# Optimization experiments

Hardware: AMD Instinct MI355X
Metric: run time of the kernel (lower is better)

## Reference

```python
import jax, jax.numpy as jnp
import numpy as np

N, D = 2048, 1024
OUT = 65536
S = 16384  # number of LSH-selected neurons


def setup_inputs() -> dict:
    key = jax.random.key(0)
    k1, k2, k3, k4 = jax.random.split(key, 4)
    x = jax.random.normal(k1, (N, D), dtype=jnp.float32)
    # original init: uniform(-1, 1) weights, zero bias; use randn-scale weights per spec
    weight = jax.random.normal(k2, (OUT, D), dtype=jnp.float32)
    bias = jax.random.normal(k3, (OUT,), dtype=jnp.float32)
    sample_ids = jax.random.randint(k4, (S,), 0, OUT, dtype=jnp.int64)
    return {"x": x, "weight": weight, "bias": bias, "sample_ids": sample_ids}


def reference(x, weight, bias, sample_ids):
    # Gather selected neuron rows (F.embedding equivalent)
    sample_weights = weight[sample_ids]          # [S, D]
    sample_bias = bias[sample_ids]               # [S]
    # x @ W_sel.T + b_sel  -> [N, S]
    sample_logits = jnp.einsum('nd,sd->ns', x, sample_weights) + sample_bias
    return sample_logits
```

## Files before the change

### kernel.cpp

```cpp
#include <hip/hip_runtime.h>
#include <stdint.h>


typedef __bf16 bf16x8 __attribute__((ext_vector_type(8)));
typedef float f32x4 __attribute__((ext_vector_type(4)));

#define BM 256
#define BN 256
#define BK 64

__device__ __forceinline__ ushort f2bf(float f) {
  union { float f; uint32_t u; } c; c.f = f;
  uint32_t u = c.u;
  return (ushort)((u + 0x7FFFu + ((u >> 16) & 1u)) >> 16);
}

__global__ __launch_bounds__(256) void prep_kernel(
    const float* __restrict__ x, const float* __restrict__ W,
    const float* __restrict__ bias, const int* __restrict__ ids,
    ushort* __restrict__ Wg, ushort* __restrict__ xb,
    float* __restrict__ biasg, int D, int S) {
  const int t = threadIdx.x;
  const int gblocks = S >> 3;
  if ((int)blockIdx.x < gblocks) {
    const int s0 = blockIdx.x << 3;
    if (t < 8) biasg[s0 + t] = bias[ids[s0 + t]];
#pragma unroll
    for (int r = 0; r < 8; ++r) {
      const int s = s0 + r;
      const int id = ids[s];
      float4 v = ((const float4*)(W + (size_t)id * D))[t];
      ushort4 o;
      o.x = f2bf(v.x); o.y = f2bf(v.y); o.z = f2bf(v.z); o.w = f2bf(v.w);
      ((ushort4*)(Wg + (size_t)s * D))[t] = o;
    }
  } else {
    const int i = (blockIdx.x - gblocks) * 256 + t;
    float4 v = ((const float4*)x)[i];
    ushort4 o;
    o.x = f2bf(v.x); o.y = f2bf(v.y); o.z = f2bf(v.z); o.w = f2bf(v.w);
    ((ushort4*)xb)[i] = o;
  }
}

__device__ __forceinline__ void load_lds16(const void* g, void* l) {
  __builtin_amdgcn_global_load_lds(
      (const __attribute__((address_space(1))) void*)g,
      (__attribute__((address_space(3))) void*)l, 16, 0, 0);
}

__global__ __launch_bounds__(512, 2) void gemm_bt_bias(
    const ushort* __restrict__ A, const ushort* __restrict__ B,
    const float* __restrict__ biasg, float* __restrict__ C,
    int M, int S, int K) {
  __shared__ __align__(16) ushort As[2 * BM * BK];
  __shared__ __align__(16) ushort Bs[2 * BN * BK];

  const int tid  = threadIdx.x;
  const int lane = tid & 63;
  const int wave = tid >> 6;
  const int wm = (wave >> 2) * 128;
  const int wn = (wave & 3) * 64;
  const int quad = lane >> 4;
  const int l16  = lane & 15;
  const int bn = blockIdx.x;
  const int bm = blockIdx.y;

  const int srow = tid >> 3;
  const int scol = (((tid & 7) ^ (srow & 7)) << 3);
  const ushort* Asrc = A + (size_t)(bm * BM + srow) * K + scol;
  const ushort* Bsrc = B + (size_t)(bn * BN + srow) * K + scol;

  const int pc0 = ((quad ^ (l16 & 7)) << 3);
  const int pc1 = (((4 + quad) ^ (l16 & 7)) << 3);

  f32x4 acc[8][4] = {};

  auto stage_tile = [&](const ushort* src, ushort* dst, int kt) {
#pragma unroll
    for (int j = 0; j < 4; ++j)
      load_lds16(src + (size_t)(j * 64) * K + kt, dst + (j * 512 + tid) * 8);
  };

  auto load_af = [&](const ushort* Acur, int ih, bf16x8 (&af)[4][2]) {
#pragma unroll
    for (int i = 0; i < 4; ++i) {
      const int ro = (wm + (ih * 4 + i) * 16 + l16) * BK;
      af[i][0] = *(const bf16x8*)(Acur + ro + pc0);
      af[i][1] = *(const bf16x8*)(Acur + ro + pc1);
    }
  };
  auto load_bq = [&](const ushort* Bcur, int jh, bf16x8 (&bq)[2][2]) {
#pragma unroll
    for (int j = 0; j < 2; ++j) {
      const int ro = (wn + (jh * 2 + j) * 16 + l16) * BK;
      bq[j][0] = *(const bf16x8*)(Bcur + ro + pc0);
      bq[j][1] = *(const bf16x8*)(Bcur + ro + pc1);
    }
  };
  auto mma_q = [&](bf16x8 (&af)[4][2], bf16x8 (&bq)[2][2], int ih, int jh) {
    __builtin_amdgcn_s_setprio(1);
#pragma unroll
    for (int ks = 0; ks < 2; ++ks)
#pragma unroll
      for (int i = 0; i < 4; ++i)
#pragma unroll
        for (int j = 0; j < 2; ++j)
          acc[ih * 4 + i][jh * 2 + j] =
              __builtin_amdgcn_mfma_f32_16x16x32_bf16(
                  af[i][ks], bq[j][ks], acc[ih * 4 + i][jh * 2 + j], 0, 0, 0);
    __builtin_amdgcn_s_setprio(0);
  };

  stage_tile(Asrc, (ushort*)As, 0);
  stage_tile(Bsrc, (ushort*)Bs, 0);

  const int NT = K / BK;
  for (int t = 0; t < NT; ++t) {
    const int cur = t & 1;
    const ushort* Acur = (const ushort*)As + cur * (BM * BK);
    const ushort* Bcur = (const ushort*)Bs + cur * (BN * BK);
    ushort* Anx = (ushort*)As + (cur ^ 1) * (BM * BK);
    ushort* Bnx = (ushort*)Bs + (cur ^ 1) * (BN * BK);
    const int kn = (t + 1) * BK;

    if (t + 1 < NT) {
      stage_tile(Asrc, Anx, kn);
      asm volatile("s_waitcnt vmcnt(4)" ::: "memory");
    } else {
      asm volatile("s_waitcnt vmcnt(0)" ::: "memory");
    }
    __builtin_amdgcn_sched_barrier(0);
    __builtin_amdgcn_s_barrier();
    __builtin_amdgcn_sched_barrier(0);

    bf16x8 af[4][2], bq0[2][2], bq1[2][2];
    load_af(Acur, 0, af);
    load_bq(Bcur, 0, bq0);
    mma_q(af, bq0, 0, 0);

    if (t + 1 < NT) stage_tile(Bsrc, Bnx, kn);
    load_bq(Bcur, 1, bq1);
    mma_q(af, bq1, 0, 1);

    load_af(Acur, 1, af);
    mma_q(af, bq1, 1, 1);

    load_bq(Bcur, 0, bq0);
    mma_q(af, bq0, 1, 0);

    __builtin_amdgcn_sched_barrier(0);
    __builtin_amdgcn_s_barrier();
    __builtin_amdgcn_sched_barrier(0);
  }

  const int row0 = bm * BM + wm + quad * 4;
  const int col0 = bn * BN + wn + l16;
#pragma unroll
  for (int jf = 0; jf < 4; ++jf) {
    const int col = col0 + jf * 16;
    const float bv = biasg[col];
#pragma unroll
    for (int i = 0; i < 8; ++i) {
#pragma unroll
      for (int r = 0; r < 4; ++r) {
        C[(size_t)(row0 + i * 16 + r) * S + col] = acc[i][jf][r] + bv;
      }
    }
  }
}

extern "C" void kernel_launch(void* const* d_in, const int* in_sizes, int n_in,
                              void* d_out, int out_size, void* d_ws, size_t ws_size,
                              hipStream_t stream) {
  const float* x    = (const float*)d_in[0];
  const float* W    = (const float*)d_in[1];
  const float* bias = (const float*)d_in[2];
  const int*   ids  = (const int*)d_in[3];
  float* out = (float*)d_out;

  const int OUTN = in_sizes[2];
  const int S    = in_sizes[3];
  const int D    = in_sizes[1] / OUTN;
  const int N    = in_sizes[0] / D;

  ushort* Wg = (ushort*)d_ws;
  ushort* xb = (ushort*)((char*)d_ws + (size_t)S * D * sizeof(ushort));
  float* biasg = (float*)((char*)d_ws + (size_t)S * D * sizeof(ushort)
                          + (size_t)N * D * sizeof(ushort));

  const int gather_blocks = S / 8;
  const int conv_blocks = (N * D) / 1024;
  prep_kernel<<<gather_blocks + conv_blocks, 256, 0, stream>>>(
      x, W, bias, ids, Wg, xb, biasg, D, S);

  dim3 grid(S / BN, N / BM);
  gemm_bt_bias<<<grid, 512, 0, stream>>>(xb, Wg, biasg, out, N, S, D);
}
```

Measured before the change: 450.4 us.

## Split K tiles into half-tiles with interleaved staging and remap blocks across XCDs

Restructures the GEMM main loop so each BK=64 tile is handled as two 32-wide K halves in four LDS half-buffers. LDS reads, async global-to-LDS staging and MFMA groups are interleaved between barriers in a ping-pong schedule, with a new swizzle layout for the narrower rows. Block IDs are also remapped so consecutive tiles land on the same XCD chunk, aiming for better L2 reuse. The cost is more barriers per K step and a more fragile schedule that depends on vmcnt accounting.

```diff
diff --git a/kernel.cpp b/kernel.cpp
--- a/kernel.cpp
+++ b/kernel.cpp
@@ -8,6 +8,8 @@
 #define BM 256
 #define BN 256
 #define BK 64
+#define KH 32
+#define HB 8192
 
 __device__ __forceinline__ ushort f2bf(float f) {
   union { float f; uint32_t u; } c; c.f = f;
@@ -49,12 +51,26 @@
       (__attribute__((address_space(3))) void*)l, 16, 0, 0);
 }
 
+#define OPEN_BAR()                                        \
+  do {                                                    \
+    __builtin_amdgcn_sched_barrier(0);                    \
+    __builtin_amdgcn_s_barrier();                         \
+    asm volatile("s_waitcnt lgkmcnt(0)" ::: "memory");    \
+    __builtin_amdgcn_sched_barrier(0);                    \
+  } while (0)
+#define CLOSE_BAR()                                       \
+  do {                                                    \
+    __builtin_amdgcn_sched_barrier(0);                    \
+    __builtin_amdgcn_s_barrier();                         \
+    __builtin_amdgcn_sched_barrier(0);                    \
+  } while (0)
+
 __global__ __launch_bounds__(512, 2) void gemm_bt_bias(
     const ushort* __restrict__ A, const ushort* __restrict__ B,
     const float* __restrict__ biasg, float* __restrict__ C,
     int M, int S, int K) {
-  __shared__ __align__(16) ushort As[2 * BM * BK];
-  __shared__ __align__(16) ushort Bs[2 * BN * BK];
+  __shared__ __align__(16) ushort As[4 * HB];
+  __shared__ __align__(16) ushort Bs[4 * HB];
 
   const int tid  = threadIdx.x;
   const int lane = tid & 63;
@@ -63,94 +79,126 @@
   const int wn = (wave & 3) * 64;
   const int quad = lane >> 4;
   const int l16  = lane & 15;
-  const int bn = blockIdx.x;
-  const int bm = blockIdx.y;
-
-  const int srow = tid >> 3;
-  const int scol = (((tid & 7) ^ (srow & 7)) << 3);
+
+  const int gx = gridDim.x;
+  int id = blockIdx.y * gx + blockIdx.x;
+  const int cpx = (gx * gridDim.y) >> 3;
+  id = (id & 7) * cpx + (id >> 3);
+  const int bn = id % gx;
+  const int bm = id / gx;
+
+  const int srow = tid >> 2;
+  const int scol = (((tid & 3) ^ ((srow >> 1) & 3)) << 3);
   const ushort* Asrc = A + (size_t)(bm * BM + srow) * K + scol;
   const ushort* Bsrc = B + (size_t)(bn * BN + srow) * K + scol;
 
-  const int pc0 = ((quad ^ (l16 & 7)) << 3);
-  const int pc1 = (((4 + quad) ^ (l16 & 7)) << 3);
+  const int rchunk = ((quad ^ ((l16 >> 1) & 3)) << 3);
 
   f32x4 acc[8][4] = {};
 
-  auto stage_tile = [&](const ushort* src, ushort* dst, int kt) {
+  auto stageA = [&](int hb, int t, int h) {
+#pragma unroll
+    for (int j = 0; j < 2; ++j)
+      load_lds16(Asrc + (size_t)(j * 128) * K + t * BK + h * KH,
+                 As + hb * HB + (j * 512 + tid) * 8);
+  };
+  auto stageB = [&](int hb, int t, int h) {
+#pragma unroll
+    for (int j = 0; j < 2; ++j)
+      load_lds16(Bsrc + (size_t)(j * 128) * K + t * BK + h * KH,
+                 Bs + hb * HB + (j * 512 + tid) * 8);
+  };
+  auto rdA = [&](bf16x8 (&a)[4], int hb, int ibase) {
+#pragma unroll
+    for (int i = 0; i < 4; ++i)
+      a[i] = *(const bf16x8*)(As + hb * HB +
+                              (wm + (ibase + i) * 16 + l16) * KH + rchunk);
+  };
+  auto rdB = [&](bf16x8 (&b)[4], int hb) {
 #pragma unroll
     for (int j = 0; j < 4; ++j)
-      load_lds16(src + (size_t)(j * 64) * K + kt, dst + (j * 512 + tid) * 8);
-  };
-
-  auto load_af = [&](const ushort* Acur, int ih, bf16x8 (&af)[4][2]) {
-#pragma unroll
-    for (int i = 0; i < 4; ++i) {
-      const int ro = (wm + (ih * 4 + i) * 16 + l16) * BK;
-      af[i][0] = *(const bf16x8*)(Acur + ro + pc0);
-      af[i][1] = *(const bf16x8*)(Acur + ro + pc1);
-    }
-  };
-  auto load_bq = [&](const ushort* Bcur, int jh, bf16x8 (&bq)[2][2]) {
-#pragma unroll
-    for (int j = 0; j < 2; ++j) {
-      const int ro = (wn + (jh * 2 + j) * 16 + l16) * BK;
-      bq[j][0] = *(const bf16x8*)(Bcur + ro + pc0);
-      bq[j][1] = *(const bf16x8*)(Bcur + ro + pc1);
-    }
-  };
-  auto mma_q = [&](bf16x8 (&af)[4][2], bf16x8 (&bq)[2][2], int ih, int jh) {
+      b[j] = *(const bf16x8*)(Bs + hb * HB + (wn + j * 16 + l16) * KH + rchunk);
+  };
+  auto mma16 = [&](bf16x8 (&a)[4], bf16x8 (&b)[4], int ibase) {
     __builtin_amdgcn_s_setprio(1);
 #pragma unroll
-    for (int ks = 0; ks < 2; ++ks)
-#pragma unroll
-      for (int i = 0; i < 4; ++i)
-#pragma unroll
-        for (int j = 0; j < 2; ++j)
-          acc[ih * 4 + i][jh * 2 + j] =
-              __builtin_amdgcn_mfma_f32_16x16x32_bf16(
-                  af[i][ks], bq[j][ks], acc[ih * 4 + i][jh * 2 + j], 0, 0, 0);
+    for (int i = 0; i < 4; ++i)
+#pragma unroll
+      for (int j = 0; j < 4; ++j)
+        acc[ibase + i][j] = __builtin_amdgcn_mfma_f32_16x16x32_bf16(
+            a[i], b[j], acc[ibase + i][j], 0, 0, 0);
     __builtin_amdgcn_s_setprio(0);
   };
 
-  stage_tile(Asrc, (ushort*)As, 0);
-  stage_tile(Bsrc, (ushort*)Bs, 0);
+  stageA(0, 0, 0); stageB(0, 0, 0); stageA(1, 0, 1); stageB(1, 0, 1);
+  __builtin_amdgcn_sched_barrier(0);
+  asm volatile("s_waitcnt vmcnt(4)" ::: "memory");
+  __builtin_amdgcn_s_barrier();
+  __builtin_amdgcn_sched_barrier(0);
 
   const int NT = K / BK;
-  for (int t = 0; t < NT; ++t) {
-    const int cur = t & 1;
-    const ushort* Acur = (const ushort*)As + cur * (BM * BK);
-    const ushort* Bcur = (const ushort*)Bs + cur * (BN * BK);
-    ushort* Anx = (ushort*)As + (cur ^ 1) * (BM * BK);
-    ushort* Bnx = (ushort*)Bs + (cur ^ 1) * (BN * BK);
-    const int kn = (t + 1) * BK;
-
-    if (t + 1 < NT) {
-      stage_tile(Asrc, Anx, kn);
-      asm volatile("s_waitcnt vmcnt(4)" ::: "memory");
-    } else {
-      asm volatile("s_waitcnt vmcnt(0)" ::: "memory");
-    }
-    __builtin_amdgcn_sched_barrier(0);
-    __builtin_amdgcn_s_barrier();
-    __builtin_amdgcn_sched_barrier(0);
-
-    bf16x8 af[4][2], bq0[2][2], bq1[2][2];
-    load_af(Acur, 0, af);
-    load_bq(Bcur, 0, bq0);
-    mma_q(af, bq0, 0, 0);
-
-    if (t + 1 < NT) stage_tile(Bsrc, Bnx, kn);
-    load_bq(Bcur, 1, bq1);
-    mma_q(af, bq1, 0, 1);
-
-    load_af(Acur, 1, af);
-    mma_q(af, bq1, 1, 1);
-
-    load_bq(Bcur, 0, bq0);
-    mma_q(af, bq0, 1, 0);
-
-    __builtin_amdgcn_sched_barrier(0);
-    __builtin_amdgcn_s_barrier();
+  bf16x8 alo[4], ahi[4], bb[4];
+
+  for (int t = 0; t < NT - 1; ++t) {
+    const int d  = (t & 1) * 2;
+    const int dn = 2 - d;
+
+    rdA(alo, d + 0, 0);
+    rdB(bb,  d + 0);
+    stageA(dn + 0, t + 1, 0);
+    OPEN_BAR();
+    mma16(alo, bb, 0);
+    CLOSE_BAR();
+
+    rdA(ahi, d + 0, 4);
+    stageB(dn + 0, t + 1, 0);
+    OPEN_BAR();
+    mma16(ahi, bb, 4);
+    __builtin_amdgcn_sched_barrier(0);
+    asm volatile("s_waitcnt vmcnt(4)" ::: "memory");
+    CLOSE_BAR();
+
+    rdA(alo, d + 1, 0);
+    rdB(bb,  d + 1);
+    stageA(dn + 1, t + 1, 1);
+    OPEN_BAR();
+    mma16(alo, bb, 0);
+    CLOSE_BAR();
+
+    rdA(ahi, d + 1, 4);
+    stageB(dn + 1, t + 1, 1);
+    OPEN_BAR();
+    mma16(ahi, bb, 4);
+    __builtin_amdgcn_sched_barrier(0);
+    asm volatile("s_waitcnt vmcnt(4)" ::: "memory");
+    CLOSE_BAR();
+  }
+
+  {
+    const int d = ((NT - 1) & 1) * 2;
+
+    rdA(alo, d + 0, 0);
+    rdB(bb,  d + 0);
+    OPEN_BAR();
+    mma16(alo, bb, 0);
+    CLOSE_BAR();
+
+    rdA(ahi, d + 0, 4);
+    OPEN_BAR();
+    mma16(ahi, bb, 4);
+    __builtin_amdgcn_sched_barrier(0);
+    asm volatile("s_waitcnt vmcnt(0)" ::: "memory");
+    CLOSE_BAR();
+
+    rdA(alo, d + 1, 0);
+    rdB(bb,  d + 1);
+    OPEN_BAR();
+    mma16(alo, bb, 0);
+    CLOSE_BAR();
+
+    rdA(ahi, d + 1, 4);
+    OPEN_BAR();
+    mma16(ahi, bb, 4);
     __builtin_amdgcn_sched_barrier(0);
   }
 
```

New measurement: 437.3 us. 2.9% less time.
